# Optimization experiments

Measured on AMD Instinct MI355X. Metric: run time of the kernel, lower is better.

Reference implementation:

```python
import jax, jax.numpy as jnp
import numpy as np

B, S, D, H = 2, 2048, 1024, 16
DEPTH = D // H


def setup_inputs() -> dict:
    key = jax.random.key(0)
    ks = jax.random.split(key, 12)
    s = 1.0 / np.sqrt(D)
    return {
        "q": jax.random.normal(ks[0], (B, S, D), jnp.float32),
        "k": jax.random.normal(ks[1], (B, S, D), jnp.float32),
        "v": jax.random.normal(ks[2], (B, S, D), jnp.float32),
        "mask": jnp.zeros((B, 1, 1, S), jnp.float32),
        "Wq": jax.random.normal(ks[3], (D, D), jnp.float32) * s,
        "bq": jnp.zeros((D,), jnp.float32),
        "Wk": jax.random.normal(ks[4], (D, D), jnp.float32) * s,
        "bk": jnp.zeros((D,), jnp.float32),
        "Wv": jax.random.normal(ks[5], (D, D), jnp.float32) * s,
        "bv": jnp.zeros((D,), jnp.float32),
        "Wo": jax.random.normal(ks[6], (D, D), jnp.float32) * s,
        "bo": jnp.zeros((D,), jnp.float32),
    }


def _split_heads(x):
    # [B, S, D] -> [B, H, S, depth]
    b, s, _ = x.shape
    return x.reshape(b, s, H, DEPTH).transpose(0, 2, 1, 3)


def reference(q, k, v, mask, Wq, bq, Wk, bk, Wv, bv, Wo, bo):
    qh = _split_heads(q @ Wq + bq)
    kh = _split_heads(k @ Wk + bk)
    vh = _split_heads(v @ Wv + bv)
    # scaled dot-product attention (TF tutorial convention: mask*-1e9 added)
    scale = 1.0 / jnp.sqrt(jnp.asarray(DEPTH, qh.dtype))
    logits = jnp.einsum("bhqd,bhkd->bhqk", qh, kh) * scale
    logits = logits + mask * jnp.asarray(-1e9, logits.dtype)
    attn = jax.nn.softmax(logits, axis=-1)  # [B,H,S,S]
    ctx = jnp.einsum("bhqk,bhkd->bhqd", attn, vh)
    ctx = ctx.transpose(0, 2, 1, 3).reshape(q.shape[0], -1, D)
    out = ctx @ Wo + bo
    return out, attn
```

## Files before the change

### kernel.cpp

```cpp
#include <hip/hip_runtime.h>
#include <math.h>

#define B_ 2
#define S_ 2048
#define D_ 1024
#define H_ 16
#define DEPTH_ 64
#define SCALE_ 0.125f


__global__ __launch_bounds__(256) void proj_kernel(
    const float* __restrict__ X, const float* __restrict__ W,
    const float* __restrict__ bias, float* __restrict__ out)
{
    __shared__ float As[16][68];
    __shared__ float Bs[16][68];
    const int tid = threadIdx.x;
    const int tx = tid & 15, ty = tid >> 4;
    const int m0 = blockIdx.y * 64;
    const int n0 = blockIdx.x * 64;
    float acc[4][4] = {};

    for (int kk = 0; kk < D_; kk += 16) {
        int idx = tid;
#pragma unroll
        for (int r = 0; r < 4; ++r, idx += 256) {
            int m = idx >> 4, k = idx & 15;
            As[k][m] = X[(size_t)(m0 + m) * D_ + kk + k];
        }
        idx = tid;
#pragma unroll
        for (int r = 0; r < 4; ++r, idx += 256) {
            int k = idx >> 6, n = idx & 63;
            Bs[k][n] = W[(size_t)(kk + k) * D_ + n0 + n];
        }
        __syncthreads();
#pragma unroll
        for (int k = 0; k < 16; ++k) {
            float4 a = *(const float4*)&As[k][ty * 4];
            float4 b = *(const float4*)&Bs[k][tx * 4];
            float av[4] = {a.x, a.y, a.z, a.w};
            float bv[4] = {b.x, b.y, b.z, b.w};
#pragma unroll
            for (int i = 0; i < 4; ++i)
#pragma unroll
                for (int j = 0; j < 4; ++j) acc[i][j] += av[i] * bv[j];
        }
        __syncthreads();
    }
#pragma unroll
    for (int i = 0; i < 4; ++i) {
        int m = m0 + ty * 4 + i;
        int b = m >> 11, s = m & 2047;
#pragma unroll
        for (int j = 0; j < 4; ++j) {
            int n = n0 + tx * 4 + j;
            int h = n >> 6, d = n & 63;
            out[((size_t)(b * H_ + h) * S_ + s) * DEPTH_ + d] = acc[i][j] + bias[n];
        }
    }
}

__global__ __launch_bounds__(256) void logits_kernel(
    const float* __restrict__ qh, const float* __restrict__ kh,
    const float* __restrict__ mask, float* __restrict__ attn)
{
    const int z = blockIdx.z;
    const int b = z >> 4;
    const float* A  = qh + (size_t)z * S_ * DEPTH_;
    const float* Bm = kh + (size_t)z * S_ * DEPTH_;
    __shared__ float As[16][68];
    __shared__ float Bs[16][68];
    const int tid = threadIdx.x;
    const int tx = tid & 15, ty = tid >> 4;
    const int m0 = blockIdx.y * 64;
    const int n0 = blockIdx.x * 64;
    float acc[4][4] = {};

    for (int kk = 0; kk < DEPTH_; kk += 16) {
        int idx = tid;
#pragma unroll
        for (int r = 0; r < 4; ++r, idx += 256) {
            int m = idx >> 4, k = idx & 15;
            As[k][m] = A [(size_t)(m0 + m) * DEPTH_ + kk + k];
            Bs[k][m] = Bm[(size_t)(n0 + m) * DEPTH_ + kk + k];
        }
        __syncthreads();
#pragma unroll
        for (int k = 0; k < 16; ++k) {
            float4 a = *(const float4*)&As[k][ty * 4];
            float4 b4 = *(const float4*)&Bs[k][tx * 4];
            float av[4] = {a.x, a.y, a.z, a.w};
            float bv[4] = {b4.x, b4.y, b4.z, b4.w};
#pragma unroll
            for (int i = 0; i < 4; ++i)
#pragma unroll
                for (int j = 0; j < 4; ++j) acc[i][j] += av[i] * bv[j];
        }
        __syncthreads();
    }
    float* C = attn + (size_t)z * S_ * S_;
#pragma unroll
    for (int i = 0; i < 4; ++i) {
        int m = m0 + ty * 4 + i;
#pragma unroll
        for (int j = 0; j < 4; ++j) {
            int n = n0 + tx * 4 + j;
            float v = acc[i][j] * SCALE_ + mask[b * S_ + n] * (-1e9f);
            C[(size_t)m * S_ + n] = v;
        }
    }
}

__global__ __launch_bounds__(256) void softmax_kernel(float* __restrict__ attn)
{
    const size_t row = blockIdx.x;
    float4* p4 = (float4*)(attn + row * S_);
    const int tid = threadIdx.x;
    const int wave = tid >> 6, lane = tid & 63;
    __shared__ float redm[4];
    __shared__ float reds[4];

    float4 x0 = p4[tid];
    float4 x1 = p4[tid + 256];
    float m = fmaxf(fmaxf(fmaxf(x0.x, x0.y), fmaxf(x0.z, x0.w)),
                    fmaxf(fmaxf(x1.x, x1.y), fmaxf(x1.z, x1.w)));
#pragma unroll
    for (int off = 32; off; off >>= 1) m = fmaxf(m, __shfl_down(m, off, 64));
    if (lane == 0) redm[wave] = m;
    __syncthreads();
    m = fmaxf(fmaxf(redm[0], redm[1]), fmaxf(redm[2], redm[3]));

    x0.x = expf(x0.x - m); x0.y = expf(x0.y - m);
    x0.z = expf(x0.z - m); x0.w = expf(x0.w - m);
    x1.x = expf(x1.x - m); x1.y = expf(x1.y - m);
    x1.z = expf(x1.z - m); x1.w = expf(x1.w - m);
    float s = x0.x + x0.y + x0.z + x0.w + x1.x + x1.y + x1.z + x1.w;
#pragma unroll
    for (int off = 32; off; off >>= 1) s += __shfl_down(s, off, 64);
    if (lane == 0) reds[wave] = s;
    __syncthreads();
    s = reds[0] + reds[1] + reds[2] + reds[3];
    float inv = 1.0f / s;
    x0.x *= inv; x0.y *= inv; x0.z *= inv; x0.w *= inv;
    x1.x *= inv; x1.y *= inv; x1.z *= inv; x1.w *= inv;
    p4[tid] = x0;
    p4[tid + 256] = x1;
}

__global__ __launch_bounds__(256) void ctx_kernel(
    const float* __restrict__ attn, const float* __restrict__ vh,
    float* __restrict__ ctx)
{
    const int z = blockIdx.z;
    const int b = z >> 4, h = z & 15;
    const float* A = attn + (size_t)z * S_ * S_;
    const float* V = vh + (size_t)z * S_ * DEPTH_;
    __shared__ float As[16][68];
    __shared__ float Bs[16][68];
    const int tid = threadIdx.x;
    const int tx = tid & 15, ty = tid >> 4;
    const int m0 = blockIdx.y * 64;
    float acc[4][4] = {};

    for (int kk = 0; kk < S_; kk += 16) {
        int idx = tid;
#pragma unroll
        for (int r = 0; r < 4; ++r, idx += 256) {
            int m = idx >> 4, k = idx & 15;
            As[k][m] = A[(size_t)(m0 + m) * S_ + kk + k];
        }
        idx = tid;
#pragma unroll
        for (int r = 0; r < 4; ++r, idx += 256) {
            int k = idx >> 6, n = idx & 63;
            Bs[k][n] = V[(size_t)(kk + k) * DEPTH_ + n];
        }
        __syncthreads();
#pragma unroll
        for (int k = 0; k < 16; ++k) {
            float4 a = *(const float4*)&As[k][ty * 4];
            float4 b4 = *(const float4*)&Bs[k][tx * 4];
            float av[4] = {a.x, a.y, a.z, a.w};
            float bv[4] = {b4.x, b4.y, b4.z, b4.w};
#pragma unroll
            for (int i = 0; i < 4; ++i)
#pragma unroll
                for (int j = 0; j < 4; ++j) acc[i][j] += av[i] * bv[j];
        }
        __syncthreads();
    }
#pragma unroll
    for (int i = 0; i < 4; ++i) {
        int s = m0 + ty * 4 + i;
#pragma unroll
        for (int j = 0; j < 4; ++j) {
            int d = tx * 4 + j;
            ctx[((size_t)(b * S_ + s)) * D_ + h * DEPTH_ + d] = acc[i][j];
        }
    }
}

__global__ __launch_bounds__(256) void out_kernel(
    const float* __restrict__ X, const float* __restrict__ W,
    const float* __restrict__ bias, float* __restrict__ out)
{
    __shared__ float As[16][68];
    __shared__ float Bs[16][68];
    const int tid = threadIdx.x;
    const int tx = tid & 15, ty = tid >> 4;
    const int m0 = blockIdx.y * 64;
    const int n0 = blockIdx.x * 64;
    float acc[4][4] = {};

    for (int kk = 0; kk < D_; kk += 16) {
        int idx = tid;
#pragma unroll
        for (int r = 0; r < 4; ++r, idx += 256) {
            int m = idx >> 4, k = idx & 15;
            As[k][m] = X[(size_t)(m0 + m) * D_ + kk + k];
        }
        idx = tid;
#pragma unroll
        for (int r = 0; r < 4; ++r, idx += 256) {
            int k = idx >> 6, n = idx & 63;
            Bs[k][n] = W[(size_t)(kk + k) * D_ + n0 + n];
        }
        __syncthreads();
#pragma unroll
        for (int k = 0; k < 16; ++k) {
            float4 a = *(const float4*)&As[k][ty * 4];
            float4 b4 = *(const float4*)&Bs[k][tx * 4];
            float av[4] = {a.x, a.y, a.z, a.w};
            float bv[4] = {b4.x, b4.y, b4.z, b4.w};
#pragma unroll
            for (int i = 0; i < 4; ++i)
#pragma unroll
                for (int j = 0; j < 4; ++j) acc[i][j] += av[i] * bv[j];
        }
        __syncthreads();
    }
#pragma unroll
    for (int i = 0; i < 4; ++i) {
        int m = m0 + ty * 4 + i;
#pragma unroll
        for (int j = 0; j < 4; ++j) {
            int n = n0 + tx * 4 + j;
            out[(size_t)m * D_ + n] = acc[i][j] + bias[n];
        }
    }
}

extern "C" void kernel_launch(void* const* d_in, const int* in_sizes, int n_in,
                              void* d_out, int out_size, void* d_ws, size_t ws_size,
                              hipStream_t stream)
{
    const float* q    = (const float*)d_in[0];
    const float* k    = (const float*)d_in[1];
    const float* v    = (const float*)d_in[2];
    const float* mask = (const float*)d_in[3];
    const float* Wq   = (const float*)d_in[4];
    const float* bq   = (const float*)d_in[5];
    const float* Wk   = (const float*)d_in[6];
    const float* bk   = (const float*)d_in[7];
    const float* Wv   = (const float*)d_in[8];
    const float* bv   = (const float*)d_in[9];
    const float* Wo   = (const float*)d_in[10];
    const float* bo   = (const float*)d_in[11];

    float* out  = (float*)d_out;
    float* attn = out + (size_t)B_ * S_ * D_;

    float* ws  = (float*)d_ws;
    float* qh  = ws;
    float* kh  = qh + (size_t)B_ * S_ * D_;
    float* vh  = kh + (size_t)B_ * S_ * D_;
    float* ctx = vh + (size_t)B_ * S_ * D_;

    dim3 blk(256);
    dim3 gproj(D_ / 64, (B_ * S_) / 64);
    proj_kernel<<<gproj, blk, 0, stream>>>(q, Wq, bq, qh);
    proj_kernel<<<gproj, blk, 0, stream>>>(k, Wk, bk, kh);
    proj_kernel<<<gproj, blk, 0, stream>>>(v, Wv, bv, vh);

    dim3 glog(S_ / 64, S_ / 64, B_ * H_);
    logits_kernel<<<glog, blk, 0, stream>>>(qh, kh, mask, attn);

    softmax_kernel<<<dim3(B_ * H_ * S_), blk, 0, stream>>>(attn);

    dim3 gctx(1, S_ / 64, B_ * H_);
    ctx_kernel<<<gctx, blk, 0, stream>>>(attn, vh, ctx);

    dim3 gout(D_ / 64, (B_ * S_) / 64);
    out_kernel<<<gout, blk, 0, stream>>>(ctx, Wo, bo, out);
}
```

Measured before the change: 1.726 ms.

## Enlarge GEMM tiles to 128x128 with 8x8 microtiles and vectorized loads

```diff
diff --git a/kernel.cpp b/kernel.cpp
--- a/kernel.cpp
+++ b/kernel.cpp
@@ -9,55 +9,74 @@
 #define SCALE_ 0.125f
 
 
-__global__ __launch_bounds__(256) void proj_kernel(
-    const float* __restrict__ X, const float* __restrict__ W,
-    const float* __restrict__ bias, float* __restrict__ out)
-{
-    __shared__ float As[16][68];
-    __shared__ float Bs[16][68];
+__global__ __launch_bounds__(256) void qkv_proj_kernel(
+    const float* __restrict__ qx, const float* __restrict__ kx,
+    const float* __restrict__ vx,
+    const float* __restrict__ Wq, const float* __restrict__ bq,
+    const float* __restrict__ Wk, const float* __restrict__ bk,
+    const float* __restrict__ Wv, const float* __restrict__ bv,
+    float* __restrict__ qh, float* __restrict__ kh, float* __restrict__ vh)
+{
+    const float* X; const float* W; const float* bias; float* out;
+    if (blockIdx.z == 0)      { X = qx; W = Wq; bias = bq; out = qh; }
+    else if (blockIdx.z == 1) { X = kx; W = Wk; bias = bk; out = kh; }
+    else                      { X = vx; W = Wv; bias = bv; out = vh; }
+
+    __shared__ float As[16][132];
+    __shared__ float Bs[16][132];
     const int tid = threadIdx.x;
     const int tx = tid & 15, ty = tid >> 4;
-    const int m0 = blockIdx.y * 64;
-    const int n0 = blockIdx.x * 64;
-    float acc[4][4] = {};
+    const int m0 = blockIdx.y * 128;
+    const int n0 = blockIdx.x * 128;
+    float acc[8][8] = {};
 
     for (int kk = 0; kk < D_; kk += 16) {
-        int idx = tid;
-#pragma unroll
-        for (int r = 0; r < 4; ++r, idx += 256) {
-            int m = idx >> 4, k = idx & 15;
-            As[k][m] = X[(size_t)(m0 + m) * D_ + kk + k];
-        }
-        idx = tid;
-#pragma unroll
-        for (int r = 0; r < 4; ++r, idx += 256) {
-            int k = idx >> 6, n = idx & 63;
-            Bs[k][n] = W[(size_t)(kk + k) * D_ + n0 + n];
+        int f = tid;
+#pragma unroll
+        for (int r = 0; r < 2; ++r, f += 256) {
+            int m = f >> 2, k4 = (f & 3) << 2;
+            float4 x = *(const float4*)&X[(size_t)(m0 + m) * D_ + kk + k4];
+            As[k4 + 0][m] = x.x; As[k4 + 1][m] = x.y;
+            As[k4 + 2][m] = x.z; As[k4 + 3][m] = x.w;
+        }
+        f = tid;
+#pragma unroll
+        for (int r = 0; r < 2; ++r, f += 256) {
+            int k = f >> 5, n4 = (f & 31) << 2;
+            *(float4*)&Bs[k][n4] = *(const float4*)&W[(size_t)(kk + k) * D_ + n0 + n4];
         }
         __syncthreads();
 #pragma unroll
         for (int k = 0; k < 16; ++k) {
-            float4 a = *(const float4*)&As[k][ty * 4];
-            float4 b = *(const float4*)&Bs[k][tx * 4];
-            float av[4] = {a.x, a.y, a.z, a.w};
-            float bv[4] = {b.x, b.y, b.z, b.w};
-#pragma unroll
-            for (int i = 0; i < 4; ++i)
-#pragma unroll
-                for (int j = 0; j < 4; ++j) acc[i][j] += av[i] * bv[j];
-        }
-        __syncthreads();
-    }
-#pragma unroll
-    for (int i = 0; i < 4; ++i) {
-        int m = m0 + ty * 4 + i;
+            float4 a0 = *(const float4*)&As[k][ty * 4];
+            float4 a1 = *(const float4*)&As[k][64 + ty * 4];
+            float4 b0 = *(const float4*)&Bs[k][tx * 4];
+            float4 b1 = *(const float4*)&Bs[k][64 + tx * 4];
+            float av[8]  = {a0.x, a0.y, a0.z, a0.w, a1.x, a1.y, a1.z, a1.w};
+            float bv8[8] = {b0.x, b0.y, b0.z, b0.w, b1.x, b1.y, b1.z, b1.w};
+#pragma unroll
+            for (int i = 0; i < 8; ++i)
+#pragma unroll
+                for (int j = 0; j < 8; ++j) acc[i][j] += av[i] * bv8[j];
+        }
+        __syncthreads();
+    }
+    float4 bl = *(const float4*)&bias[n0 + tx * 4];
+    float4 bh = *(const float4*)&bias[n0 + 64 + tx * 4];
+#pragma unroll
+    for (int ii = 0; ii < 8; ++ii) {
+        int m = m0 + ((ii >> 2) << 6) + ty * 4 + (ii & 3);
         int b = m >> 11, s = m & 2047;
-#pragma unroll
-        for (int j = 0; j < 4; ++j) {
-            int n = n0 + tx * 4 + j;
-            int h = n >> 6, d = n & 63;
-            out[((size_t)(b * H_ + h) * S_ + s) * DEPTH_ + d] = acc[i][j] + bias[n];
-        }
+        int n = n0 + tx * 4;
+        int h = n >> 6, d = n & 63;
+        float4 lo = make_float4(acc[ii][0] + bl.x, acc[ii][1] + bl.y,
+                                acc[ii][2] + bl.z, acc[ii][3] + bl.w);
+        *(float4*)&out[((size_t)(b * H_ + h) * S_ + s) * DEPTH_ + d] = lo;
+        n = n0 + 64 + tx * 4;
+        h = n >> 6; d = n & 63;
+        float4 hi = make_float4(acc[ii][4] + bh.x, acc[ii][5] + bh.y,
+                                acc[ii][6] + bh.z, acc[ii][7] + bh.w);
+        *(float4*)&out[((size_t)(b * H_ + h) * S_ + s) * DEPTH_ + d] = hi;
     }
 }
 
@@ -69,46 +88,58 @@
     const int b = z >> 4;
     const float* A  = qh + (size_t)z * S_ * DEPTH_;
     const float* Bm = kh + (size_t)z * S_ * DEPTH_;
-    __shared__ float As[16][68];
-    __shared__ float Bs[16][68];
+    __shared__ float As[16][132];
+    __shared__ float Bs[16][132];
     const int tid = threadIdx.x;
     const int tx = tid & 15, ty = tid >> 4;
-    const int m0 = blockIdx.y * 64;
-    const int n0 = blockIdx.x * 64;
-    float acc[4][4] = {};
+    const int m0 = blockIdx.y * 128;
+    const int n0 = blockIdx.x * 128;
+    float acc[8][8] = {};
 
     for (int kk = 0; kk < DEPTH_; kk += 16) {
-        int idx = tid;
-#pragma unroll
-        for (int r = 0; r < 4; ++r, idx += 256) {
-            int m = idx >> 4, k = idx & 15;
-            As[k][m] = A [(size_t)(m0 + m) * DEPTH_ + kk + k];
-            Bs[k][m] = Bm[(size_t)(n0 + m) * DEPTH_ + kk + k];
+        int f = tid;
+#pragma unroll
+        for (int r = 0; r < 2; ++r, f += 256) {
+            int m = f >> 2, k4 = (f & 3) << 2;
+            float4 x = *(const float4*)&A[(size_t)(m0 + m) * DEPTH_ + kk + k4];
+            As[k4 + 0][m] = x.x; As[k4 + 1][m] = x.y;
+            As[k4 + 2][m] = x.z; As[k4 + 3][m] = x.w;
+            float4 y = *(const float4*)&Bm[(size_t)(n0 + m) * DEPTH_ + kk + k4];
+            Bs[k4 + 0][m] = y.x; Bs[k4 + 1][m] = y.y;
+            Bs[k4 + 2][m] = y.z; Bs[k4 + 3][m] = y.w;
         }
         __syncthreads();
 #pragma unroll
         for (int k = 0; k < 16; ++k) {
-            float4 a = *(const float4*)&As[k][ty * 4];
-            float4 b4 = *(const float4*)&Bs[k][tx * 4];
-            float av[4] = {a.x, a.y, a.z, a.w};
-            float bv[4] = {b4.x, b4.y, b4.z, b4.w};
-#pragma unroll
-            for (int i = 0; i < 4; ++i)
-#pragma unroll
-                for (int j = 0; j < 4; ++j) acc[i][j] += av[i] * bv[j];
-        }
-        __syncthreads();
-    }
+            float4 a0 = *(const float4*)&As[k][ty * 4];
+            float4 a1 = *(const float4*)&As[k][64 + ty * 4];
+            float4 b0 = *(const float4*)&Bs[k][tx * 4];
+            float4 b1 = *(const float4*)&Bs[k][64 + tx * 4];
+            float av[8]  = {a0.x, a0.y, a0.z, a0.w, a1.x, a1.y, a1.z, a1.w};
+            float bv8[8] = {b0.x, b0.y, b0.z, b0.w, b1.x, b1.y, b1.z, b1.w};
+#pragma unroll
+            for (int i = 0; i < 8; ++i)
+#pragma unroll
+                for (int j = 0; j < 8; ++j) acc[i][j] += av[i] * bv8[j];
+        }
+        __syncthreads();
+    }
+    float4 ml = *(const float4*)&mask[b * S_ + n0 + tx * 4];
+    float4 mh = *(const float4*)&mask[b * S_ + n0 + 64 + tx * 4];
     float* C = attn + (size_t)z * S_ * S_;
 #pragma unroll
-    for (int i = 0; i < 4; ++i) {
-        int m = m0 + ty * 4 + i;
-#pragma unroll
-        for (int j = 0; j < 4; ++j) {
-            int n = n0 + tx * 4 + j;
-            float v = acc[i][j] * SCALE_ + mask[b * S_ + n] * (-1e9f);
-            C[(size_t)m * S_ + n] = v;
-        }
+    for (int ii = 0; ii < 8; ++ii) {
+        int m = m0 + ((ii >> 2) << 6) + ty * 4 + (ii & 3);
+        float4 lo = make_float4(acc[ii][0] * SCALE_ - 1e9f * ml.x,
+                                acc[ii][1] * SCALE_ - 1e9f * ml.y,
+                                acc[ii][2] * SCALE_ - 1e9f * ml.z,
+                                acc[ii][3] * SCALE_ - 1e9f * ml.w);
+        *(float4*)&C[(size_t)m * S_ + n0 + tx * 4] = lo;
+        float4 hi = make_float4(acc[ii][4] * SCALE_ - 1e9f * mh.x,
+                                acc[ii][5] * SCALE_ - 1e9f * mh.y,
+                                acc[ii][6] * SCALE_ - 1e9f * mh.z,
+                                acc[ii][7] * SCALE_ - 1e9f * mh.w);
+        *(float4*)&C[(size_t)m * S_ + n0 + 64 + tx * 4] = hi;
     }
 }
 
@@ -152,52 +183,50 @@
     const float* __restrict__ attn, const float* __restrict__ vh,
     float* __restrict__ ctx)
 {
-    const int z = blockIdx.z;
+    const int z = blockIdx.y;
     const int b = z >> 4, h = z & 15;
     const float* A = attn + (size_t)z * S_ * S_;
     const float* V = vh + (size_t)z * S_ * DEPTH_;
-    __shared__ float As[16][68];
+    __shared__ float As[16][132];
     __shared__ float Bs[16][68];
     const int tid = threadIdx.x;
     const int tx = tid & 15, ty = tid >> 4;
-    const int m0 = blockIdx.y * 64;
-    float acc[4][4] = {};
+    const int m0 = blockIdx.x * 128;
+    float acc[8][4] = {};
 
     for (int kk = 0; kk < S_; kk += 16) {
-        int idx = tid;
-#pragma unroll
-        for (int r = 0; r < 4; ++r, idx += 256) {
-            int m = idx >> 4, k = idx & 15;
-            As[k][m] = A[(size_t)(m0 + m) * S_ + kk + k];
-        }
-        idx = tid;
-#pragma unroll
-        for (int r = 0; r < 4; ++r, idx += 256) {
-            int k = idx >> 6, n = idx & 63;
-            Bs[k][n] = V[(size_t)(kk + k) * DEPTH_ + n];
+        int f = tid;
+#pragma unroll
+        for (int r = 0; r < 2; ++r, f += 256) {
+            int m = f >> 2, k4 = (f & 3) << 2;
+            float4 x = *(const float4*)&A[(size_t)(m0 + m) * S_ + kk + k4];
+            As[k4 + 0][m] = x.x; As[k4 + 1][m] = x.y;
+            As[k4 + 2][m] = x.z; As[k4 + 3][m] = x.w;
+        }
+        {
+            int k = tid >> 4, n4 = (tid & 15) << 2;
+            *(float4*)&Bs[k][n4] = *(const float4*)&V[(size_t)(kk + k) * DEPTH_ + n4];
         }
         __syncthreads();
 #pragma unroll
         for (int k = 0; k < 16; ++k) {
-            float4 a = *(const float4*)&As[k][ty * 4];
-            float4 b4 = *(const float4*)&Bs[k][tx * 4];
-            float av[4] = {a.x, a.y, a.z, a.w};
-            float bv[4] = {b4.x, b4.y, b4.z, b4.w};
-#pragma unroll
-            for (int i = 0; i < 4; ++i)
-#pragma unroll
-                for (int j = 0; j < 4; ++j) acc[i][j] += av[i] * bv[j];
-        }
-        __syncthreads();
-    }
-#pragma unroll
-    for (int i = 0; i < 4; ++i) {
-        int s = m0 + ty * 4 + i;
-#pragma unroll
-        for (int j = 0; j < 4; ++j) {
-            int d = tx * 4 + j;
-            ctx[((size_t)(b * S_ + s)) * D_ + h * DEPTH_ + d] = acc[i][j];
-        }
+            float4 a0 = *(const float4*)&As[k][ty * 4];
+            float4 a1 = *(const float4*)&As[k][64 + ty * 4];
+            float4 b0 = *(const float4*)&Bs[k][tx * 4];
+            float av[8]  = {a0.x, a0.y, a0.z, a0.w, a1.x, a1.y, a1.z, a1.w};
+            float bv4[4] = {b0.x, b0.y, b0.z, b0.w};
+#pragma unroll
+            for (int i = 0; i < 8; ++i)
+#pragma unroll
+                for (int j = 0; j < 4; ++j) acc[i][j] += av[i] * bv4[j];
+        }
+        __syncthreads();
+    }
+#pragma unroll
+    for (int ii = 0; ii < 8; ++ii) {
+        int s = m0 + ((ii >> 2) << 6) + ty * 4 + (ii & 3);
+        float4 r4 = make_float4(acc[ii][0], acc[ii][1], acc[ii][2], acc[ii][3]);
+        *(float4*)&ctx[((size_t)(b * S_ + s)) * D_ + h * DEPTH_ + tx * 4] = r4;
     }
 }
 
@@ -205,49 +234,56 @@
     const float* __restrict__ X, const float* __restrict__ W,
     const float* __restrict__ bias, float* __restrict__ out)
 {
-    __shared__ float As[16][68];
-    __shared__ float Bs[16][68];
+    __shared__ float As[16][132];
+    __shared__ float Bs[16][132];
     const int tid = threadIdx.x;
     const int tx = tid & 15, ty = tid >> 4;
-    const int m0 = blockIdx.y * 64;
-    const int n0 = blockIdx.x * 64;
-    float acc[4][4] = {};
+    const int m0 = blockIdx.y * 128;
+    const int n0 = blockIdx.x * 128;
+    float acc[8][8] = {};
 
     for (int kk = 0; kk < D_; kk += 16) {
-        int idx = tid;
-#pragma unroll
-        for (int r = 0; r < 4; ++r, idx += 256) {
-            int m = idx >> 4, k = idx & 15;
-            As[k][m] = X[(size_t)(m0 + m) * D_ + kk + k];
-        }
-        idx = tid;
-#pragma unroll
-        for (int r = 0; r < 4; ++r, idx += 256) {
-            int k = idx >> 6, n = idx & 63;
-            Bs[k][n] = W[(size_t)(kk + k) * D_ + n0 + n];
+        int f = tid;
+#pragma unroll
+        for (int r = 0; r < 2; ++r, f += 256) {
+            int m = f >> 2, k4 = (f & 3) << 2;
+            float4 x = *(const float4*)&X[(size_t)(m0 + m) * D_ + kk + k4];
+            As[k4 + 0][m] = x.x; As[k4 + 1][m] = x.y;
+            As[k4 + 2][m] = x.z; As[k4 + 3][m] = x.w;
+        }
+        f = tid;
+#pragma unroll
+        for (int r = 0; r < 2; ++r, f += 256) {
+            int k = f >> 5, n4 = (f & 31) << 2;
+            *(float4*)&Bs[k][n4] = *(const float4*)&W[(size_t)(kk + k) * D_ + n0 + n4];
         }
         __syncthreads();
 #pragma unroll
         for (int k = 0; k < 16; ++k) {
-            float4 a = *(const float4*)&As[k][ty * 4];
-            float4 b4 = *(const float4*)&Bs[k][tx * 4];
-            float av[4] = {a.x, a.y, a.z, a.w};
-            float bv[4] = {b4.x, b4.y, b4.z, b4.w};
-#pragma unroll
-            for (int i = 0; i < 4; ++i)
-#pragma unroll
-                for (int j = 0; j < 4; ++j) acc[i][j] += av[i] * bv[j];
-        }
-        __syncthreads();
-    }
-#pragma unroll
-    for (int i = 0; i < 4; ++i) {
-        int m = m0 + ty * 4 + i;
-#pragma unroll
-        for (int j = 0; j < 4; ++j) {
-            int n = n0 + tx * 4 + j;
-            out[(size_t)m * D_ + n] = acc[i][j] + bias[n];
-        }
+            float4 a0 = *(const float4*)&As[k][ty * 4];
+            float4 a1 = *(const float4*)&As[k][64 + ty * 4];
+            float4 b0 = *(const float4*)&Bs[k][tx * 4];
+            float4 b1 = *(const float4*)&Bs[k][64 + tx * 4];
+            float av[8]  = {a0.x, a0.y, a0.z, a0.w, a1.x, a1.y, a1.z, a1.w};
+            float bv8[8] = {b0.x, b0.y, b0.z, b0.w, b1.x, b1.y, b1.z, b1.w};
+#pragma unroll
+            for (int i = 0; i < 8; ++i)
+#pragma unroll
+                for (int j = 0; j < 8; ++j) acc[i][j] += av[i] * bv8[j];
+        }
+        __syncthreads();
+    }
+    float4 bl = *(const float4*)&bias[n0 + tx * 4];
+    float4 bh = *(const float4*)&bias[n0 + 64 + tx * 4];
+#pragma unroll
+    for (int ii = 0; ii < 8; ++ii) {
+        int m = m0 + ((ii >> 2) << 6) + ty * 4 + (ii & 3);
+        float4 lo = make_float4(acc[ii][0] + bl.x, acc[ii][1] + bl.y,
+                                acc[ii][2] + bl.z, acc[ii][3] + bl.w);
+        *(float4*)&out[(size_t)m * D_ + n0 + tx * 4] = lo;
+        float4 hi = make_float4(acc[ii][4] + bh.x, acc[ii][5] + bh.y,
+                                acc[ii][6] + bh.z, acc[ii][7] + bh.w);
+        *(float4*)&out[(size_t)m * D_ + n0 + 64 + tx * 4] = hi;
     }
 }
 
@@ -278,19 +314,15 @@
     float* ctx = vh + (size_t)B_ * S_ * D_;
 
     dim3 blk(256);
-    dim3 gproj(D_ / 64, (B_ * S_) / 64);
-    proj_kernel<<<gproj, blk, 0, stream>>>(q, Wq, bq, qh);
-    proj_kernel<<<gproj, blk, 0, stream>>>(k, Wk, bk, kh);
-    proj_kernel<<<gproj, blk, 0, stream>>>(v, Wv, bv, vh);
-
-    dim3 glog(S_ / 64, S_ / 64, B_ * H_);
-    logits_kernel<<<glog, blk, 0, stream>>>(qh, kh, mask, attn);
+
+    qkv_proj_kernel<<<dim3(8, 32, 3), blk, 0, stream>>>(
+        q, k, v, Wq, bq, Wk, bk, Wv, bv, qh, kh, vh);
+
+    logits_kernel<<<dim3(16, 16, 32), blk, 0, stream>>>(qh, kh, mask, attn);
 
     softmax_kernel<<<dim3(B_ * H_ * S_), blk, 0, stream>>>(attn);
 
-    dim3 gctx(1, S_ / 64, B_ * H_);
-    ctx_kernel<<<gctx, blk, 0, stream>>>(attn, vh, ctx);
-
-    dim3 gout(D_ / 64, (B_ * S_) / 64);
-    out_kernel<<<gout, blk, 0, stream>>>(ctx, Wo, bo, out);
-}
+    ctx_kernel<<<dim3(16, 32), blk, 0, stream>>>(attn, vh, ctx);
+
+    out_kernel<<<dim3(8, 32), blk, 0, stream>>>(ctx, Wo, bo, out);
+}
```

New measurement: 1.657 ms. 4.0% less time.
